# Performance work log

Hardware: AMD Instinct MI355X
Metric: run time of the kernel (lower is better)

Reference implementation:

```python
import jax, jax.numpy as jnp
import numpy as np

D_MODEL = 2048
N_HEAD = 16
N_KV_HEAD = 4
D_HEAD = D_MODEL // N_HEAD  # 128
WINDOW = 512
B, T = 2, 2048


def _rope_tables(T, d_head, base=10000.0):
    inv = 1.0 / (base ** (np.arange(0, d_head, 2, dtype=np.float32) / d_head))
    t = np.arange(T, dtype=np.float32)
    freqs = np.outer(t, inv)  # [T, d_head//2]
    return jnp.asarray(np.cos(freqs)), jnp.asarray(np.sin(freqs))


def setup_inputs() -> dict:
    key = jax.random.key(0)
    ks = jax.random.split(key, 5)
    cos, sin = _rope_tables(T, D_HEAD)
    s = 1.0 / np.sqrt(D_MODEL)
    return {
        "x": jax.random.normal(ks[0], (B, T, D_MODEL), jnp.float32),
        "cos": cos,
        "sin": sin,
        "Wq": jax.random.normal(ks[1], (D_MODEL, D_MODEL), jnp.float32) * s,
        "Wk": jax.random.normal(ks[2], (D_MODEL, N_KV_HEAD * D_HEAD), jnp.float32) * s,
        "Wv": jax.random.normal(ks[3], (D_MODEL, N_KV_HEAD * D_HEAD), jnp.float32) * s,
        "Wo": jax.random.normal(ks[4], (D_MODEL, D_MODEL), jnp.float32) * s,
    }


def _apply_rope(t, cos, sin):
    # t: [B, T, H, D]; cos/sin: [T, D//2]; interleaved-pair (complex) rotation
    tr = t[..., 0::2]
    ti = t[..., 1::2]
    c = cos[None, :, None, :]
    s = sin[None, :, None, :]
    out_r = tr * c - ti * s
    out_i = tr * s + ti * c
    return jnp.stack([out_r, out_i], axis=-1).reshape(t.shape)


def reference(x, cos, sin, Wq, Wk, Wv, Wo):
    Bx, Tx, C = x.shape
    q = (x @ Wq).reshape(Bx, Tx, N_HEAD, D_HEAD)       # [B,T,H,D]
    k = (x @ Wk).reshape(Bx, Tx, N_KV_HEAD, D_HEAD)    # [B,T,Hkv,D]
    v = (x @ Wv).reshape(Bx, Tx, N_KV_HEAD, D_HEAD)
    q = _apply_rope(q, cos, sin)
    k = _apply_rope(k, cos, sin)
    n_rep = N_HEAD // N_KV_HEAD
    k = jnp.repeat(k, n_rep, axis=2)  # [B,T,H,D]
    v = jnp.repeat(v, n_rep, axis=2)
    scale = 1.0 / np.sqrt(D_HEAD)
    att = jnp.einsum("bihd,bjhd->bhij", q, k) * scale  # [B,H,T,T]
    i = jnp.arange(Tx)[:, None]
    j = jnp.arange(Tx)[None, :]
    mask = (j <= i) & (j >= i - WINDOW + 1)            # causal sliding window
    att = jnp.where(mask[None, None], att, -jnp.inf)
    att = jax.nn.softmax(att, axis=-1)
    y = jnp.einsum("bhij,bjhd->bihd", att, v).reshape(Bx, Tx, C)
    return y @ Wo
```

## Files before the change

kernel.cpp:

```cpp
#include <hip/hip_runtime.h>
#include <hip/hip_bf16.h>
#include <cstdint>
#include <cstddef>

#define B_ 2
#define T_ 2048
#define NH 16
#define NKV 4
#define DH 128
#define DM 2048
#define WIN 512
#define QKS 2560

typedef __attribute__((ext_vector_type(4))) float f32x4;
typedef __attribute__((ext_vector_type(8))) __bf16 bf16x8;

using bf16 = __hip_bfloat16;

__device__ inline void gload_lds16(const void* g, void* l) {
  __builtin_amdgcn_global_load_lds(
      (const __attribute__((address_space(1))) void*)g,
      (__attribute__((address_space(3))) void*)l, 16, 0, 0);
}

__device__ inline unsigned pack_bf2(float a, float b) {
  unsigned short ua = __builtin_bit_cast(unsigned short, __float2bfloat16(a));
  unsigned short ub = __builtin_bit_cast(unsigned short, __float2bfloat16(b));
  return (unsigned)ua | ((unsigned)ub << 16);
}

#define FBAR()                           \
  do {                                   \
    asm volatile("" ::: "memory");       \
    __builtin_amdgcn_s_barrier();        \
    asm volatile("" ::: "memory");       \
  } while (0)

__global__ __launch_bounds__(256) void k_prep(const float* __restrict__ x,
                                              const float* __restrict__ Wq,
                                              const float* __restrict__ Wk,
                                              const float* __restrict__ Wv,
                                              const float* __restrict__ Wo,
                                              bf16* __restrict__ xb,
                                              bf16* __restrict__ Wqkvt,
                                              bf16* __restrict__ Wot) {
  int id = blockIdx.x;
  int tid = threadIdx.x;
  if (id >= 2560) {
    size_t base = (size_t)(id - 2560) * 4096 + tid * 16;
#pragma unroll
    for (int j = 0; j < 4; ++j) {
      float4 v = *(const float4*)(x + base + j * 4);
      ushort4 o;
      o.x = __builtin_bit_cast(unsigned short, __float2bfloat16(v.x));
      o.y = __builtin_bit_cast(unsigned short, __float2bfloat16(v.y));
      o.z = __builtin_bit_cast(unsigned short, __float2bfloat16(v.z));
      o.w = __builtin_bit_cast(unsigned short, __float2bfloat16(v.w));
      *(ushort4*)(xb + base + j * 4) = o;
    }
    return;
  }
  const float* W;
  bf16* Wt;
  int N, bx, by;
  if (id < 1024) { W = Wq; Wt = Wqkvt; N = 2048; bx = id & 31; by = id >> 5; }
  else if (id < 1280) { id -= 1024; W = Wk; Wt = Wqkvt + (size_t)2048 * 2048; N = 512; bx = id & 7; by = id >> 3; }
  else if (id < 1536) { id -= 1280; W = Wv; Wt = Wqkvt + (size_t)2560 * 2048; N = 512; bx = id & 7; by = id >> 3; }
  else { id -= 1536; W = Wo; Wt = Wot; N = 2048; bx = id & 31; by = id >> 5; }

  __shared__ float tile[64][65];
  int n0 = bx * 64, k0 = by * 64;
  int tx = tid & 63, tg = tid >> 6;
#pragma unroll
  for (int r = 0; r < 16; ++r) {
    int k = tg * 16 + r;
    tile[k][tx] = W[(size_t)(k0 + k) * N + n0 + tx];
  }
  __syncthreads();
#pragma unroll
  for (int r = 0; r < 16; ++r) {
    int nn = tg * 16 + r;
    Wt[(size_t)(n0 + nn) * 2048 + k0 + tx] = __float2bfloat16(tile[tx][nn]);
  }
}

template <int BN, int EPI>
__global__ __launch_bounds__(512, 2) void k_gemm8(const bf16* __restrict__ A,
                                                  const bf16* __restrict__ Bt,
                                                  void* __restrict__ Cout,
                                                  int M, int N, int K,
                                                  const float* __restrict__ cosT,
                                                  const float* __restrict__ sinT,
                                                  bf16* __restrict__ vt) {
  constexpr int NR = BN / 64;
  constexpr int NH0 = (NR + 1) / 2;
  constexpr int NH1 = NR - NH0;
  constexpr int VMN = 2 + NH0;
  __shared__ __align__(16) char As_[2][32768];
  __shared__ __align__(16) char Bs_[2][BN * 128];

  const int tid = threadIdx.x;
  const int w = tid >> 6, lane = tid & 63;
  const int li = lane & 15, g = lane >> 4;
  const int wm = w >> 2, wn = w & 3;

  const int nwg = gridDim.x * gridDim.y;
  int bid = blockIdx.y * gridDim.x + blockIdx.x;
  bid = (bid & 7) * (nwg >> 3) + (bid >> 3);
  const int m0 = (bid / gridDim.x) * 256;
  const int n0 = (bid % gridDim.x) * BN;

  const int ntiles = K >> 6;
  const int NT2 = ntiles >> 1;

  auto sA = [&](int buf, int tile, int half, int issue) {
    if (tile >= ntiles) return;
    const int R0 = half * 64 + issue * 128;
    const int rr = R0 + w * 8 + (lane >> 3);
    const int sl = lane & 7;
    const bf16* src = A + (size_t)(m0 + rr) * K + tile * 64 + ((sl ^ (rr & 7)) * 8);
    gload_lds16(src, As_[buf] + (R0 + w * 8) * 128);
  };
  auto sB = [&](int buf, int tile, int half, int issue) {
    if (tile >= ntiles) return;
    const int slot = issue * 8 + w;
    const int per = (half ? NH1 : NH0) * 2;
    const int wng = slot / per, within = slot % per;
    const int block = wng * (NR * 2) + (half ? NH0 * 2 : 0) + within;
    const int rr = block * 8 + (lane >> 3);
    const int sl = lane & 7;
    const bf16* src = Bt + (size_t)(n0 + rr) * K + tile * 64 + ((sl ^ (rr & 7)) * 8);
    gload_lds16(src, Bs_[buf] + block * 1024);
  };
  auto sBh = [&](int buf, int tile, int half) {
    sB(buf, tile, half, 0);
    if ((half ? NH1 : NH0) == 2) sB(buf, tile, half, 1);
  };

  const int swz0 = (g ^ (li & 7)) * 16;
  const int swz1 = ((4 + g) ^ (li & 7)) * 16;
  bf16x8 af[8], b0v[NH0 * 2], b1v[NH1 * 2];
  f32x4 acc[8][NR] = {};

  auto readA = [&](int buf, int mh) {
#pragma unroll
    for (int m = 0; m < 4; ++m) {
      const char* p = As_[buf] + (wm * 128 + mh * 64 + m * 16 + li) * 128;
      af[m * 2 + 0] = *(const bf16x8*)(p + swz0);
      af[m * 2 + 1] = *(const bf16x8*)(p + swz1);
    }
  };
  auto readB0 = [&](int buf) {
#pragma unroll
    for (int n = 0; n < NH0; ++n) {
      const char* p = Bs_[buf] + (wn * (NR * 16) + n * 16 + li) * 128;
      b0v[n * 2 + 0] = *(const bf16x8*)(p + swz0);
      b0v[n * 2 + 1] = *(const bf16x8*)(p + swz1);
    }
  };
  auto readB1 = [&](int buf) {
#pragma unroll
    for (int n = 0; n < NH1; ++n) {
      const char* p = Bs_[buf] + (wn * (NR * 16) + NH0 * 16 + n * 16 + li) * 128;
      b1v[n * 2 + 0] = *(const bf16x8*)(p + swz0);
      b1v[n * 2 + 1] = *(const bf16x8*)(p + swz1);
    }
  };
  auto MMA0 = [&](int mh) {
    __builtin_amdgcn_s_setprio(1);
#pragma unroll
    for (int m = 0; m < 4; ++m)
#pragma unroll
      for (int n = 0; n < NH0; ++n)
#pragma unroll
        for (int kk = 0; kk < 2; ++kk)
          acc[mh * 4 + m][n] = __builtin_amdgcn_mfma_f32_16x16x32_bf16(
              af[m * 2 + kk], b0v[n * 2 + kk], acc[mh * 4 + m][n], 0, 0, 0);
    __builtin_amdgcn_s_setprio(0);
  };
  auto MMA1 = [&](int mh) {
    __builtin_amdgcn_s_setprio(1);
#pragma unroll
    for (int m = 0; m < 4; ++m)
#pragma unroll
      for (int n = 0; n < NH1; ++n)
#pragma unroll
        for (int kk = 0; kk < 2; ++kk)
          acc[mh * 4 + m][NH0 + n] = __builtin_amdgcn_mfma_f32_16x16x32_bf16(
              af[m * 2 + kk], b1v[n * 2 + kk], acc[mh * 4 + m][NH0 + n], 0, 0, 0);
    __builtin_amdgcn_s_setprio(0);
  };
  auto VMW = [&](bool last) {
    if (last) {
      asm volatile("s_waitcnt vmcnt(0)" ::: "memory");
    } else {
      if constexpr (VMN == 4)
        asm volatile("s_waitcnt vmcnt(4)" ::: "memory");
      else
        asm volatile("s_waitcnt vmcnt(3)" ::: "memory");
    }
    __builtin_amdgcn_sched_barrier(0);
  };

  sA(0, 0, 0, 0); sA(0, 0, 0, 1); sA(0, 0, 1, 0); sA(0, 0, 1, 1);
  sBh(0, 0, 0); sBh(0, 0, 1);
  sA(1, 1, 0, 0); sA(1, 1, 0, 1);
  sBh(1, 1, 0);
  if constexpr (VMN == 4)
    asm volatile("s_waitcnt vmcnt(4)" ::: "memory");
  else
    asm volatile("s_waitcnt vmcnt(3)" ::: "memory");
  __builtin_amdgcn_sched_barrier(0);
  FBAR();

  for (int itr = 0; itr < NT2; ++itr) {
    const int t = itr * 2;
    const bool last = (itr == NT2 - 1);
    readA(0, 0); readB0(0);
    sA(1, t + 1, 1, 0); sA(1, t + 1, 1, 1);
    FBAR(); MMA0(0); FBAR();
    readB1(0);
    sBh(1, t + 1, 1);
    FBAR(); MMA1(0); FBAR();
    readA(0, 1);
    sA(0, t + 2, 0, 0); sA(0, t + 2, 0, 1);
    FBAR(); MMA0(1); FBAR();
    sBh(0, t + 2, 0);
    VMW(last);
    FBAR(); MMA1(1); FBAR();
    readA(1, 0); readB0(1);
    sA(0, t + 2, 1, 0); sA(0, t + 2, 1, 1);
    FBAR(); MMA0(0); FBAR();
    readB1(1);
    sBh(0, t + 2, 1);
    FBAR(); MMA1(0); FBAR();
    readA(1, 1);
    sA(1, t + 3, 0, 0); sA(1, t + 3, 0, 1);
    FBAR(); MMA0(1); FBAR();
    sBh(1, t + 3, 0);
    VMW(last);
    FBAR(); MMA1(1); FBAR();
  }

#pragma unroll
  for (int mf = 0; mf < 8; ++mf)
#pragma unroll
    for (int nf = 0; nf < NR; ++nf) {
      const int colc = n0 + wn * (NR * 16) + nf * 16;
      const int col = colc + li;
      const int row0 = m0 + wm * 128 + mf * 16 + g * 4;
      if constexpr (EPI == 2) {
        if (colc < QKS) {
          const float qs = (colc < 2048) ? 0.08838834764831845f : 1.0f;
          const int i = (col & 127) >> 1;
          const float sgn = (li & 1) ? 1.0f : -1.0f;
#pragma unroll
          for (int r = 0; r < 4; ++r) {
            const int trow = (row0 + r) & (T_ - 1);
            float v = acc[mf][nf][r];
            float pv = __shfl_xor(v, 1);
            float c = cosT[trow * 64 + i], s = sinT[trow * 64 + i];
            float o = (v * c + pv * (sgn * s)) * qs;
            ((bf16*)Cout)[(size_t)(row0 + r) * QKS + col] = __float2bfloat16(o);
          }
        } else {
          unsigned lo = pack_bf2(acc[mf][nf][0], acc[mf][nf][1]);
          unsigned hi = pack_bf2(acc[mf][nf][2], acc[mf][nf][3]);
          uint2 pk = {lo, hi};
          *(uint2*)(vt + (size_t)(col - QKS) * (B_ * T_) + row0) = pk;
        }
      } else {
#pragma unroll
        for (int r = 0; r < 4; ++r) {
          float v = acc[mf][nf][r];
          if constexpr (EPI == 1)
            ((bf16*)Cout)[(size_t)(row0 + r) * N + col] = __float2bfloat16(v);
          else
            ((float*)Cout)[(size_t)(row0 + r) * N + col] = v;
        }
      }
    }
}

__global__ __launch_bounds__(512) void k_attn(const bf16* __restrict__ qkv,
                                              const bf16* __restrict__ vt,
                                              bf16* __restrict__ Y) {
  __shared__ __align__(16) char Ks[2][9216];
  __shared__ __align__(16) char Vs[2][10240];
  __shared__ __align__(16) char Pl[8][1280];
  const int lane = threadIdx.x & 63;
  const int w = threadIdx.x >> 6;
  const int li = lane & 15, g = lane >> 4;
  const int t0 = ((int)gridDim.x - 1 - (int)blockIdx.x) * 32;
  const int b = blockIdx.y / NKV, kvh = blockIdx.y % NKV;
  const int h = kvh * 4 + (w >> 1);
  const int qrow0 = t0 + (w & 1) * 16;
  const int t = qrow0 + li;

  bf16x8 qf[4];
  const bf16* qbase = qkv + (size_t)(b * T_ + qrow0 + li) * QKS + h * DH;
#pragma unroll
  for (int dk = 0; dk < 4; ++dk) qf[dk] = *(const bf16x8*)(qbase + dk * 32 + g * 8);

  float mrow = -1e4f;
  float srow = 0.f;
  f32x4 acc[8] = {};

  int ks0 = t0 - (WIN - 1);
  if (ks0 < 0) ks0 = 0;
  ks0 &= ~31;
  const int nt = (t0 + 31 - ks0) / 32 + 1;

  const bf16* kgbase = qkv + (size_t)(b * T_) * QKS + DM + kvh * DH;
  const bf16* vgbase = vt + (size_t)(kvh * DH) * (B_ * T_) + b * T_;

  auto STAGE = [&](int buf, int kt) {
    for (int c = w; c < 19; c += 8) {
      if (c < 9) {
        int slot = c * 64 + lane;
        int row = slot / 17, cc = slot % 17;
        if (slot >= 544) { row = 0; cc = 0; }
        if (cc == 16) cc = 0;
        const bf16* src = kgbase + (size_t)(kt + row) * QKS + cc * 8;
        gload_lds16(src, Ks[buf] + c * 1024);
      } else {
        int c2 = c - 9;
        int slot = c2 * 64 + lane;
        int row = slot / 5, cc = slot % 5;
        if (cc == 4) cc = 0;
        const bf16* src = vgbase + (size_t)row * (B_ * T_) + kt + cc * 8;
        gload_lds16(src, Vs[buf] + c2 * 1024);
      }
    }
  };

  STAGE(0, ks0);
  __syncthreads();
  int cur = 0;

  for (int it = 0; it < nt; ++it) {
    const int kt = ks0 + it * 32;
    if (it + 1 < nt) STAGE(cur ^ 1, kt + 32);

    f32x4 sc[2] = {};
#pragma unroll
    for (int n = 0; n < 2; ++n)
#pragma unroll
      for (int dk = 0; dk < 4; ++dk) {
        bf16x8 kf = *(const bf16x8*)(Ks[cur] + (n * 16 + li) * 272 + dk * 64 + g * 16);
        sc[n] = __builtin_amdgcn_mfma_f32_16x16x32_bf16(kf, qf[dk], sc[n], 0, 0, 0);
      }

    float p[2][4];
    float pmax = -1e30f;
#pragma unroll
    for (int n = 0; n < 2; ++n)
#pragma unroll
      for (int r = 0; r < 4; ++r) {
        int key = kt + n * 16 + g * 4 + r;
        bool valid = (key <= t) && (key > t - WIN);
        float pv = valid ? sc[n][r] : -1e30f;
        p[n][r] = pv;
        pmax = fmaxf(pmax, pv);
      }
    pmax = fmaxf(pmax, __shfl_xor(pmax, 16));
    pmax = fmaxf(pmax, __shfl_xor(pmax, 32));

    if (!__all(pmax <= mrow)) {
      float nm = fmaxf(mrow, pmax);
      float alpha = __expf(mrow - nm);
      mrow = nm;
      srow *= alpha;
      float af_[4];
#pragma unroll
      for (int r = 0; r < 4; ++r) af_[r] = __shfl(alpha, (g << 2) + r);
#pragma unroll
      for (int db = 0; db < 8; ++db)
#pragma unroll
        for (int r = 0; r < 4; ++r) acc[db][r] *= af_[r];
    }

    float rs = 0.f;
#pragma unroll
    for (int n = 0; n < 2; ++n)
#pragma unroll
      for (int r = 0; r < 4; ++r) {
        p[n][r] = __expf(p[n][r] - mrow);
        rs += p[n][r];
      }
    rs += __shfl_xor(rs, 16);
    rs += __shfl_xor(rs, 32);
    srow += rs;

#pragma unroll
    for (int n = 0; n < 2; ++n) {
      *(unsigned*)(Pl[w] + li * 80 + n * 32 + g * 8) = pack_bf2(p[n][0], p[n][1]);
      *(unsigned*)(Pl[w] + li * 80 + n * 32 + g * 8 + 4) = pack_bf2(p[n][2], p[n][3]);
    }

    bf16x8 pf = *(const bf16x8*)(Pl[w] + li * 80 + g * 16);
#pragma unroll
    for (int db = 0; db < 8; ++db) {
      bf16x8 vf = *(const bf16x8*)(Vs[cur] + (db * 16 + li) * 80 + g * 16);
      acc[db] = __builtin_amdgcn_mfma_f32_16x16x32_bf16(pf, vf, acc[db], 0, 0, 0);
    }

    __syncthreads();
    cur ^= 1;
  }

  float inv[4];
#pragma unroll
  for (int r = 0; r < 4; ++r) inv[r] = 1.f / __shfl(srow, (g << 2) + r);
  bf16* ybase = Y + (size_t)(b * T_ + qrow0 + (g << 2)) * DM + h * DH;
#pragma unroll
  for (int r = 0; r < 4; ++r)
#pragma unroll
    for (int db = 0; db < 8; ++db)
      ybase[(size_t)r * DM + db * 16 + li] = __float2bfloat16(acc[db][r] * inv[r]);
}

extern "C" void kernel_launch(void* const* d_in, const int* in_sizes, int n_in,
                              void* d_out, int out_size, void* d_ws, size_t ws_size,
                              hipStream_t stream) {
  const float* x = (const float*)d_in[0];
  const float* cosT = (const float*)d_in[1];
  const float* sinT = (const float*)d_in[2];
  const float* Wq = (const float*)d_in[3];
  const float* Wk = (const float*)d_in[4];
  const float* Wv = (const float*)d_in[5];
  const float* Wo = (const float*)d_in[6];
  float* out = (float*)d_out;

  char* ws = (char*)d_ws;
  bf16* xb = (bf16*)ws;     ws += (size_t)4096 * 2048 * 2;
  bf16* Wqkvt = (bf16*)ws;  ws += (size_t)3072 * 2048 * 2;
  bf16* Wot = (bf16*)ws;    ws += (size_t)2048 * 2048 * 2;
  bf16* qkv = (bf16*)ws;    ws += (size_t)4096 * QKS * 2;
  bf16* vt = (bf16*)ws;     ws += (size_t)512 * 4096 * 2;
  bf16* yb = xb;

  k_prep<<<4608, 256, 0, stream>>>(x, Wq, Wk, Wv, Wo, xb, Wqkvt, Wot);

  k_gemm8<192, 2><<<dim3(3072 / 192, 4096 / 256), 512, 0, stream>>>(
      xb, Wqkvt, qkv, 4096, 3072, 2048, cosT, sinT, vt);

  k_attn<<<dim3(T_ / 32, B_ * NKV), 512, 0, stream>>>(qkv, vt, yb);

  k_gemm8<128, 0><<<dim3(2048 / 128, 4096 / 256), 512, 0, stream>>>(
      yb, Wot, out, 4096, 2048, 2048, nullptr, nullptr, nullptr);
}
```

Before: 164.7 us.

## Replace eight-phase GEMM pipeline with simpler two-phase per-tile schedule

Rewrites the main GEMM loop. The old schedule split each K tile into eight phases, each interleaving half-A and half-B loads with MFMA batches. The new one loads all of B for the tile at once and runs two MMA phases per K tile, with simpler vmcnt waits. This cuts barrier count and scheduling complexity, but prefetches less finely, so global loads may overlap less with compute.

After: 156.8 us. 4.8% less time.

```diff
diff --git a/kernel.cpp b/kernel.cpp
--- a/kernel.cpp
+++ b/kernel.cpp
@@ -85,7 +85,7 @@
 }
 
 template <int BN, int EPI>
-__global__ __launch_bounds__(512, 2) void k_gemm8(const bf16* __restrict__ A,
+__global__ __launch_bounds__(512, 2) void k_gemm2(const bf16* __restrict__ A,
                                                   const bf16* __restrict__ Bt,
                                                   void* __restrict__ Cout,
                                                   int M, int N, int K,
@@ -93,9 +93,6 @@
                                                   const float* __restrict__ sinT,
                                                   bf16* __restrict__ vt) {
   constexpr int NR = BN / 64;
-  constexpr int NH0 = (NR + 1) / 2;
-  constexpr int NH1 = NR - NH0;
-  constexpr int VMN = 2 + NH0;
   __shared__ __align__(16) char As_[2][32768];
   __shared__ __align__(16) char Bs_[2][BN * 128];
 
@@ -111,7 +108,6 @@
   const int n0 = (bid % gridDim.x) * BN;
 
   const int ntiles = K >> 6;
-  const int NT2 = ntiles >> 1;
 
   auto sA = [&](int buf, int tile, int half, int issue) {
     if (tile >= ntiles) return;
@@ -121,25 +117,18 @@
     const bf16* src = A + (size_t)(m0 + rr) * K + tile * 64 + ((sl ^ (rr & 7)) * 8);
     gload_lds16(src, As_[buf] + (R0 + w * 8) * 128);
   };
-  auto sB = [&](int buf, int tile, int half, int issue) {
+  auto sB = [&](int buf, int tile, int issue) {
     if (tile >= ntiles) return;
-    const int slot = issue * 8 + w;
-    const int per = (half ? NH1 : NH0) * 2;
-    const int wng = slot / per, within = slot % per;
-    const int block = wng * (NR * 2) + (half ? NH0 * 2 : 0) + within;
+    const int block = issue * 8 + w;
     const int rr = block * 8 + (lane >> 3);
     const int sl = lane & 7;
     const bf16* src = Bt + (size_t)(n0 + rr) * K + tile * 64 + ((sl ^ (rr & 7)) * 8);
     gload_lds16(src, Bs_[buf] + block * 1024);
   };
-  auto sBh = [&](int buf, int tile, int half) {
-    sB(buf, tile, half, 0);
-    if ((half ? NH1 : NH0) == 2) sB(buf, tile, half, 1);
-  };
 
   const int swz0 = (g ^ (li & 7)) * 16;
   const int swz1 = ((4 + g) ^ (li & 7)) * 16;
-  bf16x8 af[8], b0v[NH0 * 2], b1v[NH1 * 2];
+  bf16x8 af[8], bv[NR * 2];
   f32x4 acc[8][NR] = {};
 
   auto readA = [&](int buf, int mh) {
@@ -150,96 +139,64 @@
       af[m * 2 + 1] = *(const bf16x8*)(p + swz1);
     }
   };
-  auto readB0 = [&](int buf) {
-#pragma unroll
-    for (int n = 0; n < NH0; ++n) {
+  auto readB = [&](int buf) {
+#pragma unroll
+    for (int n = 0; n < NR; ++n) {
       const char* p = Bs_[buf] + (wn * (NR * 16) + n * 16 + li) * 128;
-      b0v[n * 2 + 0] = *(const bf16x8*)(p + swz0);
-      b0v[n * 2 + 1] = *(const bf16x8*)(p + swz1);
-    }
-  };
-  auto readB1 = [&](int buf) {
-#pragma unroll
-    for (int n = 0; n < NH1; ++n) {
-      const char* p = Bs_[buf] + (wn * (NR * 16) + NH0 * 16 + n * 16 + li) * 128;
-      b1v[n * 2 + 0] = *(const bf16x8*)(p + swz0);
-      b1v[n * 2 + 1] = *(const bf16x8*)(p + swz1);
-    }
-  };
-  auto MMA0 = [&](int mh) {
+      bv[n * 2 + 0] = *(const bf16x8*)(p + swz0);
+      bv[n * 2 + 1] = *(const bf16x8*)(p + swz1);
+    }
+  };
+  auto MMA = [&](int mh) {
     __builtin_amdgcn_s_setprio(1);
 #pragma unroll
     for (int m = 0; m < 4; ++m)
 #pragma unroll
-      for (int n = 0; n < NH0; ++n)
+      for (int n = 0; n < NR; ++n)
 #pragma unroll
         for (int kk = 0; kk < 2; ++kk)
           acc[mh * 4 + m][n] = __builtin_amdgcn_mfma_f32_16x16x32_bf16(
-              af[m * 2 + kk], b0v[n * 2 + kk], acc[mh * 4 + m][n], 0, 0, 0);
+              af[m * 2 + kk], bv[n * 2 + kk], acc[mh * 4 + m][n], 0, 0, 0);
     __builtin_amdgcn_s_setprio(0);
   };
-  auto MMA1 = [&](int mh) {
-    __builtin_amdgcn_s_setprio(1);
-#pragma unroll
-    for (int m = 0; m < 4; ++m)
-#pragma unroll
-      for (int n = 0; n < NH1; ++n)
-#pragma unroll
-        for (int kk = 0; kk < 2; ++kk)
-          acc[mh * 4 + m][NH0 + n] = __builtin_amdgcn_mfma_f32_16x16x32_bf16(
-              af[m * 2 + kk], b1v[n * 2 + kk], acc[mh * 4 + m][NH0 + n], 0, 0, 0);
-    __builtin_amdgcn_s_setprio(0);
-  };
-  auto VMW = [&](bool last) {
-    if (last) {
+  auto VMWA = [&](bool last) {
+    if (last)
       asm volatile("s_waitcnt vmcnt(0)" ::: "memory");
-    } else {
-      if constexpr (VMN == 4)
-        asm volatile("s_waitcnt vmcnt(4)" ::: "memory");
-      else
-        asm volatile("s_waitcnt vmcnt(3)" ::: "memory");
-    }
+    else if constexpr (NR == 3)
+      asm volatile("s_waitcnt vmcnt(5)" ::: "memory");
+    else
+      asm volatile("s_waitcnt vmcnt(4)" ::: "memory");
     __builtin_amdgcn_sched_barrier(0);
   };
-
-  sA(0, 0, 0, 0); sA(0, 0, 0, 1); sA(0, 0, 1, 0); sA(0, 0, 1, 1);
-  sBh(0, 0, 0); sBh(0, 0, 1);
-  sA(1, 1, 0, 0); sA(1, 1, 0, 1);
-  sBh(1, 1, 0);
-  if constexpr (VMN == 4)
-    asm volatile("s_waitcnt vmcnt(4)" ::: "memory");
-  else
-    asm volatile("s_waitcnt vmcnt(3)" ::: "memory");
+  auto VMWB = [&](bool last) {
+    if (last)
+      asm volatile("s_waitcnt vmcnt(0)" ::: "memory");
+    else
+      asm volatile("s_waitcnt vmcnt(2)" ::: "memory");
+    __builtin_amdgcn_sched_barrier(0);
+  };
+
+  sA(0, 0, 0, 0); sA(0, 0, 0, 1);
+#pragma unroll
+  for (int i = 0; i < NR; ++i) sB(0, 0, i);
+  sA(0, 0, 1, 0); sA(0, 0, 1, 1);
+  asm volatile("s_waitcnt vmcnt(2)" ::: "memory");
   __builtin_amdgcn_sched_barrier(0);
   FBAR();
 
-  for (int itr = 0; itr < NT2; ++itr) {
-    const int t = itr * 2;
-    const bool last = (itr == NT2 - 1);
-    readA(0, 0); readB0(0);
-    sA(1, t + 1, 1, 0); sA(1, t + 1, 1, 1);
-    FBAR(); MMA0(0); FBAR();
-    readB1(0);
-    sBh(1, t + 1, 1);
-    FBAR(); MMA1(0); FBAR();
-    readA(0, 1);
-    sA(0, t + 2, 0, 0); sA(0, t + 2, 0, 1);
-    FBAR(); MMA0(1); FBAR();
-    sBh(0, t + 2, 0);
-    VMW(last);
-    FBAR(); MMA1(1); FBAR();
-    readA(1, 0); readB0(1);
-    sA(0, t + 2, 1, 0); sA(0, t + 2, 1, 1);
-    FBAR(); MMA0(0); FBAR();
-    readB1(1);
-    sBh(0, t + 2, 1);
-    FBAR(); MMA1(0); FBAR();
-    readA(1, 1);
-    sA(1, t + 3, 0, 0); sA(1, t + 3, 0, 1);
-    FBAR(); MMA0(1); FBAR();
-    sBh(1, t + 3, 0);
-    VMW(last);
-    FBAR(); MMA1(1); FBAR();
+  for (int t = 0; t < ntiles; ++t) {
+    const int cb = t & 1;
+    const bool last = (t == ntiles - 1);
+    readA(cb, 0); readB(cb);
+    sA(cb ^ 1, t + 1, 0, 0); sA(cb ^ 1, t + 1, 0, 1);
+#pragma unroll
+    for (int i = 0; i < NR; ++i) sB(cb ^ 1, t + 1, i);
+    VMWA(last);
+    FBAR(); MMA(0); FBAR();
+    readA(cb, 1);
+    sA(cb ^ 1, t + 1, 1, 0); sA(cb ^ 1, t + 1, 1, 1);
+    VMWB(last);
+    FBAR(); MMA(1); FBAR();
   }
 
 #pragma unroll
@@ -442,11 +399,11 @@
 
   k_prep<<<4608, 256, 0, stream>>>(x, Wq, Wk, Wv, Wo, xb, Wqkvt, Wot);
 
-  k_gemm8<192, 2><<<dim3(3072 / 192, 4096 / 256), 512, 0, stream>>>(
+  k_gemm2<192, 2><<<dim3(3072 / 192, 4096 / 256), 512, 0, stream>>>(
       xb, Wqkvt, qkv, 4096, 3072, 2048, cosT, sinT, vt);
 
   k_attn<<<dim3(T_ / 32, B_ * NKV), 512, 0, stream>>>(qkv, vt, yb);
 
-  k_gemm8<128, 0><<<dim3(2048 / 128, 4096 / 256), 512, 0, stream>>>(
+  k_gemm2<128, 0><<<dim3(2048 / 128, 4096 / 256), 512, 0, stream>>>(
       yb, Wot, out, 4096, 2048, 2048, nullptr, nullptr, nullptr);
 }
```

## Unify GEMMs on 256x256 tiles with explicit LDS waits and rebalanced prefetch

Applied to the files above, without the earlier changes.

Replaces the templated BN GEMM with a fixed 256x256 tile kernel for both the QKV and output projections. The global-to-LDS prefetch schedule is reordered so A and B halves are spread evenly across the MMA phases, with explicit lgkmcnt waits before each MFMA group. This aims to raise data reuse per block and to better overlap loads with compute. In exchange it reduces the grid to 192 and 128 workgroups, which risks underfilling the GPU's CUs.

Measured after the change: 182.8 us. +11.0%, slower.

```diff
diff --git a/kernel.cpp b/kernel.cpp
--- a/kernel.cpp
+++ b/kernel.cpp
@@ -34,6 +34,18 @@
     asm volatile("" ::: "memory");       \
     __builtin_amdgcn_s_barrier();        \
     asm volatile("" ::: "memory");       \
+  } while (0)
+
+#define LGKM0()                                            \
+  do {                                                     \
+    asm volatile("s_waitcnt lgkmcnt(0)" ::: "memory");     \
+    __builtin_amdgcn_sched_barrier(0);                     \
+  } while (0)
+
+#define LGKM8()                                            \
+  do {                                                     \
+    asm volatile("s_waitcnt lgkmcnt(8)" ::: "memory");     \
+    __builtin_amdgcn_sched_barrier(0);                     \
   } while (0)
 
 __global__ __launch_bounds__(256) void k_prep(const float* __restrict__ x,
@@ -84,20 +96,16 @@
   }
 }
 
-template <int BN, int EPI>
-__global__ __launch_bounds__(512, 2) void k_gemm8(const bf16* __restrict__ A,
-                                                  const bf16* __restrict__ Bt,
-                                                  void* __restrict__ Cout,
-                                                  int M, int N, int K,
-                                                  const float* __restrict__ cosT,
-                                                  const float* __restrict__ sinT,
-                                                  bf16* __restrict__ vt) {
-  constexpr int NR = BN / 64;
-  constexpr int NH0 = (NR + 1) / 2;
-  constexpr int NH1 = NR - NH0;
-  constexpr int VMN = 2 + NH0;
+template <int EPI>
+__global__ __launch_bounds__(512, 2) void k_g8(const bf16* __restrict__ A,
+                                               const bf16* __restrict__ Bt,
+                                               void* __restrict__ Cout,
+                                               int M, int N, int K,
+                                               const float* __restrict__ cosT,
+                                               const float* __restrict__ sinT,
+                                               bf16* __restrict__ vt) {
   __shared__ __align__(16) char As_[2][32768];
-  __shared__ __align__(16) char Bs_[2][BN * 128];
+  __shared__ __align__(16) char Bs_[2][32768];
 
   const int tid = threadIdx.x;
   const int w = tid >> 6, lane = tid & 63;
@@ -108,7 +116,7 @@
   int bid = blockIdx.y * gridDim.x + blockIdx.x;
   bid = (bid & 7) * (nwg >> 3) + (bid >> 3);
   const int m0 = (bid / gridDim.x) * 256;
-  const int n0 = (bid % gridDim.x) * BN;
+  const int n0 = (bid % gridDim.x) * 256;
 
   const int ntiles = K >> 6;
   const int NT2 = ntiles >> 1;
@@ -123,10 +131,8 @@
   };
   auto sB = [&](int buf, int tile, int half, int issue) {
     if (tile >= ntiles) return;
-    const int slot = issue * 8 + w;
-    const int per = (half ? NH1 : NH0) * 2;
-    const int wng = slot / per, within = slot % per;
-    const int block = wng * (NR * 2) + (half ? NH0 * 2 : 0) + within;
+    const int bb = issue * 8 + w;
+    const int block = (bb >> 2) * 8 + (bb & 3) + half * 4;
     const int rr = block * 8 + (lane >> 3);
     const int sl = lane & 7;
     const bf16* src = Bt + (size_t)(n0 + rr) * K + tile * 64 + ((sl ^ (rr & 7)) * 8);
@@ -134,13 +140,17 @@
   };
   auto sBh = [&](int buf, int tile, int half) {
     sB(buf, tile, half, 0);
-    if ((half ? NH1 : NH0) == 2) sB(buf, tile, half, 1);
+    sB(buf, tile, half, 1);
+  };
+  auto sAh = [&](int buf, int tile, int half) {
+    sA(buf, tile, half, 0);
+    sA(buf, tile, half, 1);
   };
 
   const int swz0 = (g ^ (li & 7)) * 16;
   const int swz1 = ((4 + g) ^ (li & 7)) * 16;
-  bf16x8 af[8], b0v[NH0 * 2], b1v[NH1 * 2];
-  f32x4 acc[8][NR] = {};
+  bf16x8 af[8], bv0[4], bv1[4];
+  f32x4 acc[8][4] = {};
 
   auto readA = [&](int buf, int mh) {
 #pragma unroll
@@ -152,18 +162,18 @@
   };
   auto readB0 = [&](int buf) {
 #pragma unroll
-    for (int n = 0; n < NH0; ++n) {
-      const char* p = Bs_[buf] + (wn * (NR * 16) + n * 16 + li) * 128;
-      b0v[n * 2 + 0] = *(const bf16x8*)(p + swz0);
-      b0v[n * 2 + 1] = *(const bf16x8*)(p + swz1);
+    for (int n = 0; n < 2; ++n) {
+      const char* p = Bs_[buf] + (wn * 64 + n * 16 + li) * 128;
+      bv0[n * 2 + 0] = *(const bf16x8*)(p + swz0);
+      bv0[n * 2 + 1] = *(const bf16x8*)(p + swz1);
     }
   };
   auto readB1 = [&](int buf) {
 #pragma unroll
-    for (int n = 0; n < NH1; ++n) {
-      const char* p = Bs_[buf] + (wn * (NR * 16) + NH0 * 16 + n * 16 + li) * 128;
-      b1v[n * 2 + 0] = *(const bf16x8*)(p + swz0);
-      b1v[n * 2 + 1] = *(const bf16x8*)(p + swz1);
+    for (int n = 0; n < 2; ++n) {
+      const char* p = Bs_[buf] + (wn * 64 + 32 + n * 16 + li) * 128;
+      bv1[n * 2 + 0] = *(const bf16x8*)(p + swz0);
+      bv1[n * 2 + 1] = *(const bf16x8*)(p + swz1);
     }
   };
   auto MMA0 = [&](int mh) {
@@ -171,11 +181,11 @@
 #pragma unroll
     for (int m = 0; m < 4; ++m)
 #pragma unroll
-      for (int n = 0; n < NH0; ++n)
+      for (int n = 0; n < 2; ++n)
 #pragma unroll
         for (int kk = 0; kk < 2; ++kk)
           acc[mh * 4 + m][n] = __builtin_amdgcn_mfma_f32_16x16x32_bf16(
-              af[m * 2 + kk], b0v[n * 2 + kk], acc[mh * 4 + m][n], 0, 0, 0);
+              af[m * 2 + kk], bv0[n * 2 + kk], acc[mh * 4 + m][n], 0, 0, 0);
     __builtin_amdgcn_s_setprio(0);
   };
   auto MMA1 = [&](int mh) {
@@ -183,61 +193,53 @@
 #pragma unroll
     for (int m = 0; m < 4; ++m)
 #pragma unroll
-      for (int n = 0; n < NH1; ++n)
+      for (int n = 0; n < 2; ++n)
 #pragma unroll
         for (int kk = 0; kk < 2; ++kk)
-          acc[mh * 4 + m][NH0 + n] = __builtin_amdgcn_mfma_f32_16x16x32_bf16(
-              af[m * 2 + kk], b1v[n * 2 + kk], acc[mh * 4 + m][NH0 + n], 0, 0, 0);
+          acc[mh * 4 + m][2 + n] = __builtin_amdgcn_mfma_f32_16x16x32_bf16(
+              af[m * 2 + kk], bv1[n * 2 + kk], acc[mh * 4 + m][2 + n], 0, 0, 0);
     __builtin_amdgcn_s_setprio(0);
   };
-  auto VMW = [&](bool last) {
-    if (last) {
+  auto VMW = [&](bool drain) {
+    if (drain)
       asm volatile("s_waitcnt vmcnt(0)" ::: "memory");
-    } else {
-      if constexpr (VMN == 4)
-        asm volatile("s_waitcnt vmcnt(4)" ::: "memory");
-      else
-        asm volatile("s_waitcnt vmcnt(3)" ::: "memory");
-    }
+    else
+      asm volatile("s_waitcnt vmcnt(6)" ::: "memory");
     __builtin_amdgcn_sched_barrier(0);
   };
 
-  sA(0, 0, 0, 0); sA(0, 0, 0, 1); sA(0, 0, 1, 0); sA(0, 0, 1, 1);
-  sBh(0, 0, 0); sBh(0, 0, 1);
-  sA(1, 1, 0, 0); sA(1, 1, 0, 1);
-  sBh(1, 1, 0);
-  if constexpr (VMN == 4)
-    asm volatile("s_waitcnt vmcnt(4)" ::: "memory");
-  else
-    asm volatile("s_waitcnt vmcnt(3)" ::: "memory");
-  __builtin_amdgcn_sched_barrier(0);
+  sAh(0, 0, 0); sBh(0, 0, 0); sBh(0, 0, 1); sAh(0, 0, 1);
+  sAh(1, 1, 0); sBh(1, 1, 0); sBh(1, 1, 1);
+  VMW(false);
   FBAR();
 
   for (int itr = 0; itr < NT2; ++itr) {
     const int t = itr * 2;
     const bool last = (itr == NT2 - 1);
     readA(0, 0); readB0(0);
-    sA(1, t + 1, 1, 0); sA(1, t + 1, 1, 1);
-    FBAR(); MMA0(0); FBAR();
+    sAh(1, t + 1, 1);
+    LGKM8();
+    FBAR(); LGKM0(); MMA0(0); FBAR();
     readB1(0);
-    sBh(1, t + 1, 1);
-    FBAR(); MMA1(0); FBAR();
+    sAh(0, t + 2, 0);
+    FBAR(); LGKM0(); MMA1(0); FBAR();
     readA(0, 1);
-    sA(0, t + 2, 0, 0); sA(0, t + 2, 0, 1);
-    FBAR(); MMA0(1); FBAR();
     sBh(0, t + 2, 0);
+    FBAR(); LGKM0(); MMA0(1); FBAR();
+    sBh(0, t + 2, 1);
     VMW(last);
     FBAR(); MMA1(1); FBAR();
     readA(1, 0); readB0(1);
-    sA(0, t + 2, 1, 0); sA(0, t + 2, 1, 1);
-    FBAR(); MMA0(0); FBAR();
+    sAh(0, t + 2, 1);
+    LGKM8();
+    FBAR(); LGKM0(); MMA0(0); FBAR();
     readB1(1);
-    sBh(0, t + 2, 1);
-    FBAR(); MMA1(0); FBAR();
+    sAh(1, t + 3, 0);
+    FBAR(); LGKM0(); MMA1(0); FBAR();
     readA(1, 1);
-    sA(1, t + 3, 0, 0); sA(1, t + 3, 0, 1);
-    FBAR(); MMA0(1); FBAR();
     sBh(1, t + 3, 0);
+    FBAR(); LGKM0(); MMA0(1); FBAR();
+    sBh(1, t + 3, 1);
     VMW(last);
     FBAR(); MMA1(1); FBAR();
   }
@@ -245,8 +247,8 @@
 #pragma unroll
   for (int mf = 0; mf < 8; ++mf)
 #pragma unroll
-    for (int nf = 0; nf < NR; ++nf) {
-      const int colc = n0 + wn * (NR * 16) + nf * 16;
+    for (int nf = 0; nf < 4; ++nf) {
+      const int colc = n0 + wn * 64 + nf * 16;
       const int col = colc + li;
       const int row0 = m0 + wm * 128 + mf * 16 + g * 4;
       if constexpr (EPI == 2) {
@@ -271,13 +273,8 @@
         }
       } else {
 #pragma unroll
-        for (int r = 0; r < 4; ++r) {
-          float v = acc[mf][nf][r];
-          if constexpr (EPI == 1)
-            ((bf16*)Cout)[(size_t)(row0 + r) * N + col] = __float2bfloat16(v);
-          else
-            ((float*)Cout)[(size_t)(row0 + r) * N + col] = v;
-        }
+        for (int r = 0; r < 4; ++r)
+          ((float*)Cout)[(size_t)(row0 + r) * N + col] = acc[mf][nf][r];
       }
     }
 }
@@ -442,11 +439,11 @@
 
   k_prep<<<4608, 256, 0, stream>>>(x, Wq, Wk, Wv, Wo, xb, Wqkvt, Wot);
 
-  k_gemm8<192, 2><<<dim3(3072 / 192, 4096 / 256), 512, 0, stream>>>(
+  k_g8<2><<<dim3(3072 / 256, 4096 / 256), 512, 0, stream>>>(
       xb, Wqkvt, qkv, 4096, 3072, 2048, cosT, sinT, vt);
 
   k_attn<<<dim3(T_ / 32, B_ * NKV), 512, 0, stream>>>(qkv, vt, yb);
 
-  k_gemm8<128, 0><<<dim3(2048 / 128, 4096 / 256), 512, 0, stream>>>(
+  k_g8<0><<<dim3(2048 / 256, 4096 / 256), 512, 0, stream>>>(
       yb, Wot, out, 4096, 2048, 2048, nullptr, nullptr, nullptr);
 }
```
